# Performance work log

Hardware: AMD Instinct MI355X
Metric: run time of the kernel (lower is better)

Reference implementation:

```python
import jax, jax.numpy as jnp
import numpy as np

# Forest of complete binary trees modeling query plans.
B = 512          # number of plans (trees)
D = 11           # tree depth; leaves at level D-1
LEAVES = 1 << (D - 1)      # 1024 leaves per tree
N_INT = LEAVES - 1         # 1023 internal nodes per tree (BFS heap order)
F_LEAF = 64      # leaf ('Scan') feature dim
F_INT = 32       # internal operator feature dim
H = 128          # hidden_dim
NHID = 4         # num_layers=5 -> input layer + 4 hidden layers
DV = 32          # data_vec_dim
OUT = 1 + DV     # latency + data vector


def _mlp(x, W_in, b_in, W_hid, b_hid, W_out, b_out):
    """GenericUnit: Linear+ReLU input layer, NHID Linear+ReLU hidden layers, linear output."""
    h = jax.nn.relu(x @ W_in + b_in)
    for i in range(W_hid.shape[0]):  # small fixed loop over layers
        h = jax.nn.relu(h @ W_hid[i] + b_hid[i])
    return h @ W_out + b_out


def setup_inputs() -> dict:
    key = jax.random.key(0)
    ks = jax.random.split(key, 8)

    def w(k, shape, fan_in):
        return jax.random.normal(k, shape, jnp.float32) * np.float32(1.0 / np.sqrt(fan_in))

    return {
        "leaf_feat": jax.random.normal(ks[0], (B, LEAVES, F_LEAF), jnp.float32),
        "int_feat": jax.random.normal(ks[1], (B, N_INT, F_INT), jnp.float32),
        # leaf unit (0 children)
        "leaf_W_in": w(ks[2], (F_LEAF, H), F_LEAF),
        "leaf_b_in": jnp.zeros((H,), jnp.float32),
        "leaf_W_hid": w(ks[3], (NHID, H, H), H),
        "leaf_b_hid": jnp.zeros((NHID, H), jnp.float32),
        "leaf_W_out": w(ks[4], (H, OUT), H),
        "leaf_b_out": jnp.zeros((OUT,), jnp.float32),
        # internal unit (2 children): input = F_INT + 2*OUT = 98
        "int_W_in": w(ks[5], (F_INT + 2 * OUT, H), F_INT + 2 * OUT),
        "int_b_in": jnp.zeros((H,), jnp.float32),
        "int_W_hid": w(ks[6], (NHID, H, H), H),
        "int_b_hid": jnp.zeros((NHID, H), jnp.float32),
        "int_W_out": w(ks[7], (H, OUT), H),
        "int_b_out": jnp.zeros((OUT,), jnp.float32),
    }


def reference(leaf_feat, int_feat,
              leaf_W_in, leaf_b_in, leaf_W_hid, leaf_b_hid, leaf_W_out, leaf_b_out,
              int_W_in, int_b_in, int_W_hid, int_b_hid, int_W_out, int_b_out):
    # Leaves (level D-1): [B, LEAVES, OUT]
    cur = _mlp(leaf_feat, leaf_W_in, leaf_b_in, leaf_W_hid, leaf_b_hid, leaf_W_out, leaf_b_out)
    # Bottom-up over internal levels; level d has 2^d nodes at BFS offsets [2^d-1, 2^(d+1)-1)
    for d in range(D - 2, -1, -1):
        n = 1 << d
        feats = int_feat[:, n - 1: 2 * n - 1, :]            # [B, n, F_INT]
        children = cur.reshape(B, n, 2 * OUT)               # concat of two child outputs
        unit_in = jnp.concatenate([feats, children], axis=-1)
        cur = _mlp(unit_in, int_W_in, int_b_in, int_W_hid, int_b_hid, int_W_out, int_b_out)
    # Root output, latency channel: [B]
    return cur[:, 0, 0]
```

## Files before the change

kernel.cpp:

```cpp
#include <hip/hip_runtime.h>
#include <cstdint>
#include <cstddef>

constexpr int Bn     = 512;
constexpr int Dd     = 11;
constexpr int LEAVES = 1024;
constexpr int NINT   = 1023;
constexpr int FLEAF  = 64;
constexpr int FINT   = 32;
constexpr int Hh     = 128;
constexpr int OUTC   = 33;

#define THREADS  256
#define WTHREADS 512
constexpr int KSTR  = 136;
constexpr int MATSZ = 128 * KSTR;

using short8 = __attribute__((ext_vector_type(8))) short;
using f32x4  = __attribute__((ext_vector_type(4))) float;

__device__ __forceinline__ unsigned int f2bf_rne_u(float f) {
  unsigned int u = __float_as_uint(f);
  u += 0x7fffu + ((u >> 16) & 1);
  return u;
}
__device__ __forceinline__ unsigned short f2bf_rne(float f) {
  return (unsigned short)(f2bf_rne_u(f) >> 16);
}
__device__ __forceinline__ float bf2f(unsigned short h) {
  return __uint_as_float((unsigned int)h << 16);
}
__device__ __forceinline__ float trunc_bf(float a) {
  return __uint_as_float(__float_as_uint(a) & 0xffff0000u);
}
__device__ __forceinline__ unsigned int pack_hi_trunc(float a, float b) {
  return __builtin_amdgcn_perm(__float_as_uint(b), __float_as_uint(a), 0x07060302u);
}
__device__ __forceinline__ unsigned int pack_lo_rne(float a, float b) {
  unsigned int r;
  asm("v_cvt_pk_bf16_f32 %0, %1, %2" : "=v"(r) : "v"(a), "v"(b));
  return r;
}

template <int KC>
__device__ __forceinline__ void dense_layer(
    unsigned short* Ah, unsigned short* Al,
    const unsigned short* __restrict__ WTh, const unsigned short* __restrict__ WTl,
    const float* __restrict__ bias)
{
  const int tid  = threadIdx.x;
  const int wave = tid >> 6;
  const int lane = tid & 63;
  const int quad = lane >> 4;
  const int l16  = lane & 15;
  const int nbase = (wave & 3) * 32;
  const int rbase = (wave >> 2) * 64;

  short8 wh[2][KC];
#pragma unroll
  for (int nt = 0; nt < 2; ++nt) {
    const int n = nbase + nt * 16 + l16;
#pragma unroll
    for (int kc = 0; kc < KC; ++kc)
      wh[nt][kc] = *(const short8*)&WTh[n * KSTR + kc * 32 + quad * 8];
  }
  float4 bv[2];
#pragma unroll
  for (int nt = 0; nt < 2; ++nt)
    bv[nt] = *(const float4*)&bias[nbase + nt * 16 + quad * 4];

  f32x4 c[4][2];
#pragma unroll
  for (int mt = 0; mt < 4; ++mt)
#pragma unroll
    for (int nt = 0; nt < 2; ++nt) c[mt][nt] = (f32x4){0.f, 0.f, 0.f, 0.f};

#pragma unroll
  for (int kc = 0; kc < KC; ++kc) {
    const int k0 = kc * 32 + quad * 8;
    short8 wl[2];
#pragma unroll
    for (int nt = 0; nt < 2; ++nt) {
      const int n = nbase + nt * 16 + l16;
      wl[nt] = *(const short8*)&WTl[n * KSTR + k0];
    }
    short8 ah[4], al[4];
#pragma unroll
    for (int mt = 0; mt < 4; ++mt) {
      ah[mt] = *(const short8*)&Ah[(rbase + mt * 16 + l16) * KSTR + k0];
      al[mt] = *(const short8*)&Al[(rbase + mt * 16 + l16) * KSTR + k0];
    }
#pragma unroll
    for (int mt = 0; mt < 4; ++mt)
#pragma unroll
      for (int nt = 0; nt < 2; ++nt)
        c[mt][nt] = __builtin_amdgcn_mfma_f32_16x16x32_bf16(wh[nt][kc], ah[mt], c[mt][nt], 0, 0, 0);
#pragma unroll
    for (int mt = 0; mt < 4; ++mt)
#pragma unroll
      for (int nt = 0; nt < 2; ++nt)
        c[mt][nt] = __builtin_amdgcn_mfma_f32_16x16x32_bf16(wh[nt][kc], al[mt], c[mt][nt], 0, 0, 0);
#pragma unroll
    for (int mt = 0; mt < 4; ++mt)
#pragma unroll
      for (int nt = 0; nt < 2; ++nt)
        c[mt][nt] = __builtin_amdgcn_mfma_f32_16x16x32_bf16(wl[nt], ah[mt], c[mt][nt], 0, 0, 0);
  }
  __syncthreads();

#pragma unroll
  for (int mt = 0; mt < 4; ++mt) {
    const int m = rbase + mt * 16 + l16;
#pragma unroll
    for (int nt = 0; nt < 2; ++nt) {
      const int nb = nbase + nt * 16 + quad * 4;
      float v0 = fmaxf(c[mt][nt][0] + bv[nt].x, 0.f);
      float v1 = fmaxf(c[mt][nt][1] + bv[nt].y, 0.f);
      float v2 = fmaxf(c[mt][nt][2] + bv[nt].z, 0.f);
      float v3 = fmaxf(c[mt][nt][3] + bv[nt].w, 0.f);
      const unsigned int h0 = pack_hi_trunc(v0, v1);
      const unsigned int h1 = pack_hi_trunc(v2, v3);
      const unsigned int l0 = pack_lo_rne(v0 - trunc_bf(v0), v1 - trunc_bf(v1));
      const unsigned int l1 = pack_lo_rne(v2 - trunc_bf(v2), v3 - trunc_bf(v3));
      *(uint2*)&Ah[m * KSTR + nb] = make_uint2(h0, h1);
      *(uint2*)&Al[m * KSTR + nb] = make_uint2(l0, l1);
    }
  }
  __syncthreads();
}

__device__ __forceinline__ void out_layer(
    const unsigned short* Ah, const unsigned short* Al,
    const unsigned short* __restrict__ WTh, const unsigned short* __restrict__ WTl,
    const float* __restrict__ bias,
    unsigned short* outH, unsigned short* outL, float* finalOut)
{
  const int tid  = threadIdx.x;
  const int wave = tid >> 6;
  const int w3   = wave & 3;
  const int rbase = (wave >> 2) * 64;
  const int lane = tid & 63;
  const int quad = lane >> 4;
  const int l16  = lane & 15;
  if (w3 < 3) {
    const int n_row = w3 * 16 + l16;
    short8 wh[4], wl[4];
#pragma unroll
    for (int kc = 0; kc < 4; ++kc) {
      wh[kc] = *(const short8*)&WTh[n_row * KSTR + kc * 32 + quad * 8];
      wl[kc] = *(const short8*)&WTl[n_row * KSTR + kc * 32 + quad * 8];
    }
    const int nb = w3 * 16 + quad * 4;
    const float4 bv = *(const float4*)&bias[nb];
    const float bvr[4] = {bv.x, bv.y, bv.z, bv.w};

    f32x4 c[4];
#pragma unroll
    for (int mt = 0; mt < 4; ++mt) c[mt] = (f32x4){0.f, 0.f, 0.f, 0.f};
#pragma unroll
    for (int kc = 0; kc < 4; ++kc) {
      const int k0 = kc * 32 + quad * 8;
#pragma unroll
      for (int mt = 0; mt < 4; ++mt) {
        const short8 ah = *(const short8*)&Ah[(rbase + mt * 16 + l16) * KSTR + k0];
        const short8 al = *(const short8*)&Al[(rbase + mt * 16 + l16) * KSTR + k0];
        c[mt] = __builtin_amdgcn_mfma_f32_16x16x32_bf16(wh[kc], ah, c[mt], 0, 0, 0);
        c[mt] = __builtin_amdgcn_mfma_f32_16x16x32_bf16(wh[kc], al, c[mt], 0, 0, 0);
        c[mt] = __builtin_amdgcn_mfma_f32_16x16x32_bf16(wl[kc], ah, c[mt], 0, 0, 0);
      }
    }
#pragma unroll
    for (int mt = 0; mt < 4; ++mt) {
      const int m = rbase + mt * 16 + l16;
#pragma unroll
      for (int r = 0; r < 4; ++r) {
        const int n = nb + r;
        const float v = c[mt][r] + bvr[r];
        if (n < OUTC) {
          outH[m * 33 + n] = (unsigned short)(__float_as_uint(v) >> 16);
          outL[m * 33 + n] = f2bf_rne(v - trunc_bf(v));
        }
        if (finalOut && n == 0) finalOut[m] = v;
      }
    }
  }
}

__global__ __launch_bounds__(WTHREADS, 4)
void leaf_kernel(const float* __restrict__ X,
                 const unsigned short* __restrict__ warena,
                 const float* __restrict__ barena,
                 unsigned short* __restrict__ outH, unsigned short* __restrict__ outL)
{
  __shared__ unsigned short Ah[128 * KSTR];
  __shared__ unsigned short Al[128 * KSTR];
  const int row_base = blockIdx.x * 128;
  const int tid = threadIdx.x;

#pragma unroll
  for (int j = 0; j < 4; ++j) {
    const int e  = tid + j * WTHREADS;
    const int r  = e >> 4;
    const int k0 = (e & 15) << 2;
    const float4 v = *(const float4*)&X[(size_t)(row_base + r) * FLEAF + k0];
    const unsigned int h0 = pack_hi_trunc(v.x, v.y);
    const unsigned int h1 = pack_hi_trunc(v.z, v.w);
    const unsigned int l0 = pack_lo_rne(v.x - trunc_bf(v.x), v.y - trunc_bf(v.y));
    const unsigned int l1 = pack_lo_rne(v.z - trunc_bf(v.z), v.w - trunc_bf(v.w));
    *(uint2*)&Ah[r * KSTR + k0] = make_uint2(h0, h1);
    *(uint2*)&Al[r * KSTR + k0] = make_uint2(l0, l1);
  }
  __syncthreads();

  dense_layer<2>(Ah, Al, warena + 0 * 2 * MATSZ, warena + 0 * 2 * MATSZ + MATSZ, barena + 0 * 128);
#pragma unroll
  for (int l = 0; l < 4; ++l) {
    const int id = 1 + l;
    dense_layer<4>(Ah, Al, warena + id * 2 * MATSZ, warena + id * 2 * MATSZ + MATSZ, barena + id * 128);
  }
  out_layer(Ah, Al, warena + 5 * 2 * MATSZ, warena + 5 * 2 * MATSZ + MATSZ, barena + 5 * 128,
            outH + (size_t)row_base * 33, outL + (size_t)row_base * 33, nullptr);
}

__global__ __launch_bounds__(WTHREADS, 4)
void int_kernel(const float* __restrict__ feat,
                const unsigned short* __restrict__ prevH, const unsigned short* __restrict__ prevL,
                const unsigned short* __restrict__ warena, const float* __restrict__ barena,
                unsigned short* __restrict__ outH, unsigned short* __restrict__ outL,
                float* __restrict__ finalOut,
                int n, int logn)
{
  __shared__ unsigned short Ah[128 * KSTR];
  __shared__ unsigned short Al[128 * KSTR];
  const int tid = threadIdx.x;
  const int m = tid & 127;
  const int g = tid >> 7;
  const int row = blockIdx.x * 128 + m;
  const int b = row >> logn;
  const int i = row & (n - 1);

  const float* fr = feat + ((size_t)b * NINT + (n - 1) + i) * FINT;
#pragma unroll
  for (int j = 0; j < 4; ++j) {
    const int cch = g + 4 * j;
    const float2 v = *(const float2*)&fr[cch * 2];
    *(unsigned int*)&Ah[m * KSTR + cch * 2] = pack_hi_trunc(v.x, v.y);
    *(unsigned int*)&Al[m * KSTR + cch * 2] = pack_lo_rne(v.x - trunc_bf(v.x), v.y - trunc_bf(v.y));
  }
  const size_t c0 = ((size_t)b * (n << 1) + (i << 1)) * 33;
#pragma unroll
  for (int j = 0; j < 9; ++j) {
    const int p = g + 4 * j;
    if (p < 33) {
      const unsigned int hv = *(const unsigned int*)&prevH[c0 + 2 * p];
      const unsigned int lv = *(const unsigned int*)&prevL[c0 + 2 * p];
      *(unsigned int*)&Ah[m * KSTR + 32 + 2 * p] = hv;
      *(unsigned int*)&Al[m * KSTR + 32 + 2 * p] = lv;
    }
  }
#pragma unroll
  for (int j = 0; j < 4; ++j) {
    const int p = g + 4 * j;
    if (p < 15) {
      *(unsigned int*)&Ah[m * KSTR + 98 + 2 * p] = 0u;
      *(unsigned int*)&Al[m * KSTR + 98 + 2 * p] = 0u;
    }
  }
  __syncthreads();

  dense_layer<4>(Ah, Al, warena + 6 * 2 * MATSZ, warena + 6 * 2 * MATSZ + MATSZ, barena + 6 * 128);
#pragma unroll
  for (int l = 0; l < 4; ++l) {
    const int id = 7 + l;
    dense_layer<4>(Ah, Al, warena + id * 2 * MATSZ, warena + id * 2 * MATSZ + MATSZ, barena + id * 128);
  }
  out_layer(Ah, Al, warena + 11 * 2 * MATSZ, warena + 11 * 2 * MATSZ + MATSZ, barena + 11 * 128,
            outH + (size_t)blockIdx.x * 128 * 33, outL + (size_t)blockIdx.x * 128 * 33,
            finalOut ? (finalOut + blockIdx.x * 128) : nullptr);
}

__global__ void prep_kernel(const float* __restrict__ lW_in, const float* __restrict__ lW_hid,
                            const float* __restrict__ lW_out, const float* __restrict__ lb_in,
                            const float* __restrict__ lb_hid, const float* __restrict__ lb_out,
                            const float* __restrict__ iW_in, const float* __restrict__ iW_hid,
                            const float* __restrict__ iW_out, const float* __restrict__ ib_in,
                            const float* __restrict__ ib_hid, const float* __restrict__ ib_out,
                            unsigned short* __restrict__ warena, float* __restrict__ barena)
{
  const int id = blockIdx.y;
  const float* W; const float* bs; int K, N;
  if (id == 0)       { W = lW_in;                        bs = lb_in;                 K = FLEAF; N = Hh; }
  else if (id <= 4)  { W = lW_hid + (id - 1) * Hh * Hh;  bs = lb_hid + (id - 1) * Hh; K = Hh;   N = Hh; }
  else if (id == 5)  { W = lW_out;                       bs = lb_out;                K = Hh;    N = OUTC; }
  else if (id == 6)  { W = iW_in;                        bs = ib_in;                 K = FINT + 2 * OUTC; N = Hh; }
  else if (id <= 10) { W = iW_hid + (id - 7) * Hh * Hh;  bs = ib_hid + (id - 7) * Hh; K = Hh;   N = Hh; }
  else               { W = iW_out;                       bs = ib_out;                K = Hh;    N = OUTC; }

  unsigned short* dh = warena + id * 2 * MATSZ;
  unsigned short* dl = dh + MATSZ;
  const int e = blockIdx.x * THREADS + threadIdx.x;
  if (e < MATSZ) {
    const int nn = e / KSTR;
    const int kk = e - nn * KSTR;
    const float v = (kk < K && nn < N) ? W[(size_t)kk * N + nn] : 0.f;
    const unsigned short h = f2bf_rne(v);
    dh[e] = h;
    dl[e] = f2bf_rne(v - bf2f(h));
  }
  if (blockIdx.x == 0 && threadIdx.x < 128)
    barena[id * 128 + threadIdx.x] = (threadIdx.x < N) ? bs[threadIdx.x] : 0.f;
}

extern "C" void kernel_launch(void* const* d_in, const int* in_sizes, int n_in,
                              void* d_out, int out_size, void* d_ws, size_t ws_size,
                              hipStream_t stream) {
  const float* leaf_feat = (const float*)d_in[0];
  const float* int_feat  = (const float*)d_in[1];
  const float* lW_in  = (const float*)d_in[2];
  const float* lb_in  = (const float*)d_in[3];
  const float* lW_hid = (const float*)d_in[4];
  const float* lb_hid = (const float*)d_in[5];
  const float* lW_out = (const float*)d_in[6];
  const float* lb_out = (const float*)d_in[7];
  const float* iW_in  = (const float*)d_in[8];
  const float* ib_in  = (const float*)d_in[9];
  const float* iW_hid = (const float*)d_in[10];
  const float* ib_hid = (const float*)d_in[11];
  const float* iW_out = (const float*)d_in[12];
  const float* ib_out = (const float*)d_in[13];
  float* out = (float*)d_out;

  const size_t rowsA = (size_t)Bn * LEAVES;
  const size_t rowsB = rowsA / 2;
  unsigned short* AH = (unsigned short*)d_ws;
  unsigned short* AL = AH + rowsA * 33;
  unsigned short* BH = AL + rowsA * 33;
  unsigned short* BL = BH + rowsB * 33;
  unsigned short* warena = BL + rowsB * 33;
  float* barena = (float*)(warena + 24 * MATSZ);

  prep_kernel<<<dim3((MATSZ + THREADS - 1) / THREADS, 12), THREADS, 0, stream>>>(
      lW_in, lW_hid, lW_out, lb_in, lb_hid, lb_out,
      iW_in, iW_hid, iW_out, ib_in, ib_hid, ib_out, warena, barena);

  leaf_kernel<<<(Bn * LEAVES) / 128, WTHREADS, 0, stream>>>(leaf_feat, warena, barena, AH, AL);

  int_kernel<<<2048, WTHREADS, 0, stream>>>(int_feat, AH, AL, warena, barena, BH, BL, nullptr, 512, 9);
  int_kernel<<<1024, WTHREADS, 0, stream>>>(int_feat, BH, BL, warena, barena, AH, AL, nullptr, 256, 8);
  int_kernel<<< 512, WTHREADS, 0, stream>>>(int_feat, AH, AL, warena, barena, BH, BL, nullptr, 128, 7);
  int_kernel<<< 256, WTHREADS, 0, stream>>>(int_feat, BH, BL, warena, barena, AH, AL, nullptr,  64, 6);
  int_kernel<<< 128, WTHREADS, 0, stream>>>(int_feat, AH, AL, warena, barena, BH, BL, nullptr,  32, 5);
  int_kernel<<<  64, WTHREADS, 0, stream>>>(int_feat, BH, BL, warena, barena, AH, AL, nullptr,  16, 4);
  int_kernel<<<  32, WTHREADS, 0, stream>>>(int_feat, AH, AL, warena, barena, BH, BL, nullptr,   8, 3);
  int_kernel<<<  16, WTHREADS, 0, stream>>>(int_feat, BH, BL, warena, barena, AH, AL, nullptr,   4, 2);
  int_kernel<<<   8, WTHREADS, 0, stream>>>(int_feat, AH, AL, warena, barena, BH, BL, nullptr,   2, 1);
  int_kernel<<<   4, WTHREADS, 0, stream>>>(int_feat, BH, BL, warena, barena, AH, AL, out,        1, 0);
}
```

Before: 968.4 us.

## Shrink row tile to 32 rows per block with 2-wave column split

Reduces each block from 128 rows with 8 waves to 32 rows with 2 waves. Each wave now owns 64 output columns over all 32 rows, and it streams weight fragments per k-chunk instead of keeping them in registers. Launch grids grow fourfold, which gives more blocks for the small upper tree levels and uses less LDS per block. In exchange, weights are reloaded more often relative to the rows computed, and each weight load is reused across fewer rows.

```diff
diff --git a/kernel.cpp b/kernel.cpp
--- a/kernel.cpp
+++ b/kernel.cpp
@@ -12,7 +12,7 @@
 constexpr int OUTC   = 33;
 
 #define THREADS  256
-#define WTHREADS 512
+#define WTHREADS 128
 constexpr int KSTR  = 136;
 constexpr int MATSZ = 128 * KSTR;
 
@@ -53,66 +53,61 @@
   const int lane = tid & 63;
   const int quad = lane >> 4;
   const int l16  = lane & 15;
-  const int nbase = (wave & 3) * 32;
-  const int rbase = (wave >> 2) * 64;
-
-  short8 wh[2][KC];
-#pragma unroll
-  for (int nt = 0; nt < 2; ++nt) {
-    const int n = nbase + nt * 16 + l16;
-#pragma unroll
-    for (int kc = 0; kc < KC; ++kc)
-      wh[nt][kc] = *(const short8*)&WTh[n * KSTR + kc * 32 + quad * 8];
-  }
-  float4 bv[2];
-#pragma unroll
-  for (int nt = 0; nt < 2; ++nt)
-    bv[nt] = *(const float4*)&bias[nbase + nt * 16 + quad * 4];
-
-  f32x4 c[4][2];
-#pragma unroll
-  for (int mt = 0; mt < 4; ++mt)
-#pragma unroll
-    for (int nt = 0; nt < 2; ++nt) c[mt][nt] = (f32x4){0.f, 0.f, 0.f, 0.f};
+  const int nbase = wave * 64;
+
+  f32x4 c[2][4];
+#pragma unroll
+  for (int mt = 0; mt < 2; ++mt)
+#pragma unroll
+    for (int nt = 0; nt < 4; ++nt) c[mt][nt] = (f32x4){0.f, 0.f, 0.f, 0.f};
 
 #pragma unroll
   for (int kc = 0; kc < KC; ++kc) {
     const int k0 = kc * 32 + quad * 8;
-    short8 wl[2];
-#pragma unroll
-    for (int nt = 0; nt < 2; ++nt) {
-      const int n = nbase + nt * 16 + l16;
-      wl[nt] = *(const short8*)&WTl[n * KSTR + k0];
-    }
-    short8 ah[4], al[4];
-#pragma unroll
-    for (int mt = 0; mt < 4; ++mt) {
-      ah[mt] = *(const short8*)&Ah[(rbase + mt * 16 + l16) * KSTR + k0];
-      al[mt] = *(const short8*)&Al[(rbase + mt * 16 + l16) * KSTR + k0];
-    }
-#pragma unroll
-    for (int mt = 0; mt < 4; ++mt)
-#pragma unroll
-      for (int nt = 0; nt < 2; ++nt)
-        c[mt][nt] = __builtin_amdgcn_mfma_f32_16x16x32_bf16(wh[nt][kc], ah[mt], c[mt][nt], 0, 0, 0);
-#pragma unroll
-    for (int mt = 0; mt < 4; ++mt)
-#pragma unroll
-      for (int nt = 0; nt < 2; ++nt)
-        c[mt][nt] = __builtin_amdgcn_mfma_f32_16x16x32_bf16(wh[nt][kc], al[mt], c[mt][nt], 0, 0, 0);
-#pragma unroll
-    for (int mt = 0; mt < 4; ++mt)
-#pragma unroll
-      for (int nt = 0; nt < 2; ++nt)
-        c[mt][nt] = __builtin_amdgcn_mfma_f32_16x16x32_bf16(wl[nt], ah[mt], c[mt][nt], 0, 0, 0);
+    short8 ah[2], al[2];
+#pragma unroll
+    for (int mt = 0; mt < 2; ++mt) {
+      ah[mt] = *(const short8*)&Ah[(mt * 16 + l16) * KSTR + k0];
+      al[mt] = *(const short8*)&Al[(mt * 16 + l16) * KSTR + k0];
+    }
+#pragma unroll
+    for (int np = 0; np < 2; ++np) {
+      short8 wh[2], wl[2];
+#pragma unroll
+      for (int j = 0; j < 2; ++j) {
+        const int n = nbase + (np * 2 + j) * 16 + l16;
+        wh[j] = *(const short8*)&WTh[n * KSTR + k0];
+        wl[j] = *(const short8*)&WTl[n * KSTR + k0];
+      }
+#pragma unroll
+      for (int mt = 0; mt < 2; ++mt)
+#pragma unroll
+        for (int j = 0; j < 2; ++j)
+          c[mt][np * 2 + j] = __builtin_amdgcn_mfma_f32_16x16x32_bf16(wh[j], ah[mt], c[mt][np * 2 + j], 0, 0, 0);
+#pragma unroll
+      for (int mt = 0; mt < 2; ++mt)
+#pragma unroll
+        for (int j = 0; j < 2; ++j)
+          c[mt][np * 2 + j] = __builtin_amdgcn_mfma_f32_16x16x32_bf16(wh[j], al[mt], c[mt][np * 2 + j], 0, 0, 0);
+#pragma unroll
+      for (int mt = 0; mt < 2; ++mt)
+#pragma unroll
+        for (int j = 0; j < 2; ++j)
+          c[mt][np * 2 + j] = __builtin_amdgcn_mfma_f32_16x16x32_bf16(wl[j], ah[mt], c[mt][np * 2 + j], 0, 0, 0);
+    }
   }
   __syncthreads();
 
-#pragma unroll
-  for (int mt = 0; mt < 4; ++mt) {
-    const int m = rbase + mt * 16 + l16;
-#pragma unroll
-    for (int nt = 0; nt < 2; ++nt) {
+  float4 bv[4];
+#pragma unroll
+  for (int nt = 0; nt < 4; ++nt)
+    bv[nt] = *(const float4*)&bias[nbase + nt * 16 + quad * 4];
+
+#pragma unroll
+  for (int mt = 0; mt < 2; ++mt) {
+    const int m = mt * 16 + l16;
+#pragma unroll
+    for (int nt = 0; nt < 4; ++nt) {
       const int nb = nbase + nt * 16 + quad * 4;
       float v0 = fmaxf(c[mt][nt][0] + bv[nt].x, 0.f);
       float v1 = fmaxf(c[mt][nt][1] + bv[nt].y, 0.f);
@@ -137,50 +132,54 @@
 {
   const int tid  = threadIdx.x;
   const int wave = tid >> 6;
-  const int w3   = wave & 3;
-  const int rbase = (wave >> 2) * 64;
   const int lane = tid & 63;
   const int quad = lane >> 4;
   const int l16  = lane & 15;
-  if (w3 < 3) {
-    const int n_row = w3 * 16 + l16;
-    short8 wh[4], wl[4];
-#pragma unroll
-    for (int kc = 0; kc < 4; ++kc) {
-      wh[kc] = *(const short8*)&WTh[n_row * KSTR + kc * 32 + quad * 8];
-      wl[kc] = *(const short8*)&WTl[n_row * KSTR + kc * 32 + quad * 8];
-    }
-    const int nb = w3 * 16 + quad * 4;
-    const float4 bv = *(const float4*)&bias[nb];
-    const float bvr[4] = {bv.x, bv.y, bv.z, bv.w};
-
-    f32x4 c[4];
-#pragma unroll
-    for (int mt = 0; mt < 4; ++mt) c[mt] = (f32x4){0.f, 0.f, 0.f, 0.f};
-#pragma unroll
-    for (int kc = 0; kc < 4; ++kc) {
-      const int k0 = kc * 32 + quad * 8;
-#pragma unroll
-      for (int mt = 0; mt < 4; ++mt) {
-        const short8 ah = *(const short8*)&Ah[(rbase + mt * 16 + l16) * KSTR + k0];
-        const short8 al = *(const short8*)&Al[(rbase + mt * 16 + l16) * KSTR + k0];
-        c[mt] = __builtin_amdgcn_mfma_f32_16x16x32_bf16(wh[kc], ah, c[mt], 0, 0, 0);
-        c[mt] = __builtin_amdgcn_mfma_f32_16x16x32_bf16(wh[kc], al, c[mt], 0, 0, 0);
-        c[mt] = __builtin_amdgcn_mfma_f32_16x16x32_bf16(wl[kc], ah, c[mt], 0, 0, 0);
+#pragma unroll
+  for (int t = 0; t < 2; ++t) {
+    const int tile = wave * 2 + t;
+    if (tile < 3) {
+      const int n_row = tile * 16 + l16;
+      f32x4 c[2];
+#pragma unroll
+      for (int mt = 0; mt < 2; ++mt) c[mt] = (f32x4){0.f, 0.f, 0.f, 0.f};
+#pragma unroll
+      for (int kc = 0; kc < 4; ++kc) {
+        const int k0 = kc * 32 + quad * 8;
+        const short8 wh = *(const short8*)&WTh[n_row * KSTR + k0];
+        const short8 wl = *(const short8*)&WTl[n_row * KSTR + k0];
+        short8 ah[2], al[2];
+#pragma unroll
+        for (int mt = 0; mt < 2; ++mt) {
+          ah[mt] = *(const short8*)&Ah[(mt * 16 + l16) * KSTR + k0];
+          al[mt] = *(const short8*)&Al[(mt * 16 + l16) * KSTR + k0];
+        }
+#pragma unroll
+        for (int mt = 0; mt < 2; ++mt)
+          c[mt] = __builtin_amdgcn_mfma_f32_16x16x32_bf16(wh, ah[mt], c[mt], 0, 0, 0);
+#pragma unroll
+        for (int mt = 0; mt < 2; ++mt)
+          c[mt] = __builtin_amdgcn_mfma_f32_16x16x32_bf16(wh, al[mt], c[mt], 0, 0, 0);
+#pragma unroll
+        for (int mt = 0; mt < 2; ++mt)
+          c[mt] = __builtin_amdgcn_mfma_f32_16x16x32_bf16(wl, ah[mt], c[mt], 0, 0, 0);
       }
-    }
-#pragma unroll
-    for (int mt = 0; mt < 4; ++mt) {
-      const int m = rbase + mt * 16 + l16;
-#pragma unroll
-      for (int r = 0; r < 4; ++r) {
-        const int n = nb + r;
-        const float v = c[mt][r] + bvr[r];
-        if (n < OUTC) {
-          outH[m * 33 + n] = (unsigned short)(__float_as_uint(v) >> 16);
-          outL[m * 33 + n] = f2bf_rne(v - trunc_bf(v));
+      const int nb = tile * 16 + quad * 4;
+      const float4 bv = *(const float4*)&bias[nb];
+      const float bvr[4] = {bv.x, bv.y, bv.z, bv.w};
+#pragma unroll
+      for (int mt = 0; mt < 2; ++mt) {
+        const int m = mt * 16 + l16;
+#pragma unroll
+        for (int r = 0; r < 4; ++r) {
+          const int n = nb + r;
+          const float v = c[mt][r] + bvr[r];
+          if (n < OUTC) {
+            outH[m * 33 + n] = (unsigned short)(__float_as_uint(v) >> 16);
+            outL[m * 33 + n] = f2bf_rne(v - trunc_bf(v));
+          }
+          if (finalOut && n == 0) finalOut[m] = v;
         }
-        if (finalOut && n == 0) finalOut[m] = v;
       }
     }
   }
@@ -192,9 +191,9 @@
                  const float* __restrict__ barena,
                  unsigned short* __restrict__ outH, unsigned short* __restrict__ outL)
 {
-  __shared__ unsigned short Ah[128 * KSTR];
-  __shared__ unsigned short Al[128 * KSTR];
-  const int row_base = blockIdx.x * 128;
+  __shared__ unsigned short Ah[32 * KSTR];
+  __shared__ unsigned short Al[32 * KSTR];
+  const int row_base = blockIdx.x * 32;
   const int tid = threadIdx.x;
 
 #pragma unroll
@@ -230,12 +229,12 @@
                 float* __restrict__ finalOut,
                 int n, int logn)
 {
-  __shared__ unsigned short Ah[128 * KSTR];
-  __shared__ unsigned short Al[128 * KSTR];
+  __shared__ unsigned short Ah[32 * KSTR];
+  __shared__ unsigned short Al[32 * KSTR];
   const int tid = threadIdx.x;
-  const int m = tid & 127;
-  const int g = tid >> 7;
-  const int row = blockIdx.x * 128 + m;
+  const int m = tid & 31;
+  const int g = tid >> 5;
+  const int row = blockIdx.x * 32 + m;
   const int b = row >> logn;
   const int i = row & (n - 1);
 
@@ -275,8 +274,8 @@
     dense_layer<4>(Ah, Al, warena + id * 2 * MATSZ, warena + id * 2 * MATSZ + MATSZ, barena + id * 128);
   }
   out_layer(Ah, Al, warena + 11 * 2 * MATSZ, warena + 11 * 2 * MATSZ + MATSZ, barena + 11 * 128,
-            outH + (size_t)blockIdx.x * 128 * 33, outL + (size_t)blockIdx.x * 128 * 33,
-            finalOut ? (finalOut + blockIdx.x * 128) : nullptr);
+            outH + (size_t)blockIdx.x * 32 * 33, outL + (size_t)blockIdx.x * 32 * 33,
+            finalOut ? (finalOut + blockIdx.x * 32) : nullptr);
 }
 
 __global__ void prep_kernel(const float* __restrict__ lW_in, const float* __restrict__ lW_hid,
@@ -343,16 +342,16 @@
       lW_in, lW_hid, lW_out, lb_in, lb_hid, lb_out,
       iW_in, iW_hid, iW_out, ib_in, ib_hid, ib_out, warena, barena);
 
-  leaf_kernel<<<(Bn * LEAVES) / 128, WTHREADS, 0, stream>>>(leaf_feat, warena, barena, AH, AL);
-
-  int_kernel<<<2048, WTHREADS, 0, stream>>>(int_feat, AH, AL, warena, barena, BH, BL, nullptr, 512, 9);
-  int_kernel<<<1024, WTHREADS, 0, stream>>>(int_feat, BH, BL, warena, barena, AH, AL, nullptr, 256, 8);
-  int_kernel<<< 512, WTHREADS, 0, stream>>>(int_feat, AH, AL, warena, barena, BH, BL, nullptr, 128, 7);
-  int_kernel<<< 256, WTHREADS, 0, stream>>>(int_feat, BH, BL, warena, barena, AH, AL, nullptr,  64, 6);
-  int_kernel<<< 128, WTHREADS, 0, stream>>>(int_feat, AH, AL, warena, barena, BH, BL, nullptr,  32, 5);
-  int_kernel<<<  64, WTHREADS, 0, stream>>>(int_feat, BH, BL, warena, barena, AH, AL, nullptr,  16, 4);
-  int_kernel<<<  32, WTHREADS, 0, stream>>>(int_feat, AH, AL, warena, barena, BH, BL, nullptr,   8, 3);
-  int_kernel<<<  16, WTHREADS, 0, stream>>>(int_feat, BH, BL, warena, barena, AH, AL, nullptr,   4, 2);
-  int_kernel<<<   8, WTHREADS, 0, stream>>>(int_feat, AH, AL, warena, barena, BH, BL, nullptr,   2, 1);
-  int_kernel<<<   4, WTHREADS, 0, stream>>>(int_feat, BH, BL, warena, barena, AH, AL, out,        1, 0);
-}
+  leaf_kernel<<<(Bn * LEAVES) / 32, WTHREADS, 0, stream>>>(leaf_feat, warena, barena, AH, AL);
+
+  int_kernel<<<8192, WTHREADS, 0, stream>>>(int_feat, AH, AL, warena, barena, BH, BL, nullptr, 512, 9);
+  int_kernel<<<4096, WTHREADS, 0, stream>>>(int_feat, BH, BL, warena, barena, AH, AL, nullptr, 256, 8);
+  int_kernel<<<2048, WTHREADS, 0, stream>>>(int_feat, AH, AL, warena, barena, BH, BL, nullptr, 128, 7);
+  int_kernel<<<1024, WTHREADS, 0, stream>>>(int_feat, BH, BL, warena, barena, AH, AL, nullptr,  64, 6);
+  int_kernel<<< 512, WTHREADS, 0, stream>>>(int_feat, AH, AL, warena, barena, BH, BL, nullptr,  32, 5);
+  int_kernel<<< 256, WTHREADS, 0, stream>>>(int_feat, BH, BL, warena, barena, AH, AL, nullptr,  16, 4);
+  int_kernel<<< 128, WTHREADS, 0, stream>>>(int_feat, AH, AL, warena, barena, BH, BL, nullptr,   8, 3);
+  int_kernel<<<  64, WTHREADS, 0, stream>>>(int_feat, BH, BL, warena, barena, AH, AL, nullptr,   4, 2);
+  int_kernel<<<  32, WTHREADS, 0, stream>>>(int_feat, AH, AL, warena, barena, BH, BL, nullptr,   2, 1);
+  int_kernel<<<  16, WTHREADS, 0, stream>>>(int_feat, BH, BL, warena, barena, AH, AL, out,        1, 0);
+}
```

After: 1.244 ms. 1.28x slower.
